# Kernel optimization log

Measured on AMD Instinct MI355X. Metric: run time of the kernel, lower is better.

Reference implementation:

```python
import jax, jax.numpy as jnp
import numpy as np

N = 4096

def setup_inputs() -> dict:
    key = jax.random.key(0)
    k1, k2, k3 = jax.random.split(key, 3)
    x = jax.random.normal(k1, (N, N), dtype=jnp.float32)
    # nn.Linear(N, N, bias=False) weight matrices, shape [out, in] = [N, N]
    s = 1.0 / np.sqrt(N)
    W_r = jax.random.uniform(k2, (N, N), dtype=jnp.float32, minval=-s, maxval=s)
    W_i = jax.random.uniform(k3, (N, N), dtype=jnp.float32, minval=-s, maxval=s)
    return {"x": x, "W_r": W_r, "W_i": W_i}

def reference(x, W_r, W_i):
    # Row pass: fft_in_rows[i] = Linear_real(x[i]) + 1j * Linear_imag(x[i])
    #   => R = x @ W_r^T + 1j * (x @ W_i^T)
    R_r = x @ W_r.T            # [N, N]
    R_i = x @ W_i.T            # [N, N]
    # Column pass: fft_in_cols[:, i] = fft_in_rows[:, i] @ (W_r + 1j W_i)
    #   => C = W^T @ R with W = W_r + 1j W_i (complex matmul in real arithmetic)
    C_r = W_r.T @ R_r - W_i.T @ R_i
    C_i = W_r.T @ R_i + W_i.T @ R_r
    # res = cat([real, imag], dim=1) -> [N, 2N]
    return jnp.concatenate([C_r, C_i], axis=1)
```

## Files before the change

kernel.cpp:

```cpp
#include <hip/hip_runtime.h>
#include <hip/hip_bf16.h>

#define NN 4096

typedef unsigned short u16;
using bf16x8 = __attribute__((ext_vector_type(8))) short;
using f32x4  = __attribute__((ext_vector_type(4))) float;
using u32x4  = __attribute__((ext_vector_type(4))) unsigned int;

__device__ inline u16 f2bf(float f) {
    union { float f; unsigned u; } c; c.f = f;
    unsigned r = (c.u + 0x7fffu + ((c.u >> 16) & 1u)) >> 16;
    return (u16)r;
}

__device__ inline void gld16(const void* g, void* l) {
    __builtin_amdgcn_global_load_lds(
        (const __attribute__((address_space(1))) void*)g,
        (__attribute__((address_space(3))) void*)l, 16, 0, 0);
}

__device__ inline bf16x8 negbf(bf16x8 v) {
    u32x4 u; __builtin_memcpy(&u, &v, 16);
    u ^= 0x80008000u;
    bf16x8 r; __builtin_memcpy(&r, &u, 16);
    return r;
}

__device__ inline void swz_tile(int bid, int& brow, int& bcol) {
    const int xcd   = bid & 7;
    const int local = bid >> 3;
    const int rr    = xcd >> 1;
    const int rc    = xcd & 1;
    brow = (rr * 8  + (local >> 4)) * 128;
    bcol = (rc * 16 + (local & 15)) * 128;
}

__global__ __launch_bounds__(256) void cvt_bf16(const float* __restrict__ s,
                                                u16* __restrict__ d) {
    size_t i = ((size_t)blockIdx.x * 256 + threadIdx.x) * 8;
    float4 v0 = *(const float4*)(s + i);
    float4 v1 = *(const float4*)(s + i + 4);
    bf16x8 o;
    o[0] = (short)f2bf(v0.x); o[1] = (short)f2bf(v0.y);
    o[2] = (short)f2bf(v0.z); o[3] = (short)f2bf(v0.w);
    o[4] = (short)f2bf(v1.x); o[5] = (short)f2bf(v1.y);
    o[6] = (short)f2bf(v1.z); o[7] = (short)f2bf(v1.w);
    *(bf16x8*)(d + i) = o;
}

__global__ __launch_bounds__(256) void tr_cvt(const float* __restrict__ s,
                                              u16* __restrict__ d) {
    __shared__ float t[32][33];
    int x  = blockIdx.x * 32 + threadIdx.x;
    int y0 = blockIdx.y * 32;
#pragma unroll
    for (int j = 0; j < 32; j += 8)
        t[threadIdx.y + j][threadIdx.x] = s[(size_t)(y0 + threadIdx.y + j) * NN + x];
    __syncthreads();
    int x2 = blockIdx.y * 32 + threadIdx.x;
    int y2 = blockIdx.x * 32;
#pragma unroll
    for (int j = 0; j < 32; j += 8)
        d[(size_t)(y2 + threadIdx.y + j) * NN + x2] = f2bf(t[threadIdx.x][threadIdx.y + j]);
}

#define P_BAR  __builtin_amdgcn_s_barrier()
#define P_LGKM do { asm volatile("s_waitcnt lgkmcnt(0)" ::: "memory"); \
                    __builtin_amdgcn_sched_barrier(0); } while (0)
#define P_VM0  do { asm volatile("s_waitcnt vmcnt(0)" ::: "memory"); \
                    __builtin_amdgcn_sched_barrier(0); } while (0)

#define CHAIN(AF, BF, ACC) do { \
    __builtin_amdgcn_s_setprio(1); \
    _Pragma("unroll") \
    for (int i_ = 0; i_ < 4; i_++) \
        _Pragma("unroll") \
        for (int j_ = 0; j_ < 4; j_++) \
            ACC[i_][j_] = __builtin_amdgcn_mfma_f32_16x16x32_bf16(AF[i_], BF[j_], ACC[i_][j_], 0, 0, 0); \
    __builtin_amdgcn_s_setprio(0); \
} while (0)

#define RD4(DST, CC, TILE, BASE) do { \
    _Pragma("unroll") \
    for (int i_ = 0; i_ < 4; i_++) \
        DST[i_] = *(const bf16x8*)&sm[CC][TILE][((BASE) + i_ * 16 + rl) * 32 + kg]; \
} while (0)


__global__ __launch_bounds__(256, 2) void gemm_pass1(
    const u16* __restrict__ Ar, const u16* __restrict__ Ai,
    const u16* __restrict__ B,
    u16* __restrict__ Cr, u16* __restrict__ Ci) {
    __shared__ u16 sm[2][3][4096];

    int brow, bcol;
    swz_tile(blockIdx.x, brow, bcol);

    const int tid  = threadIdx.x;
    const int lane = tid & 63;
    const int wid  = tid >> 6;
    const int wm   = (wid >> 1) * 64;
    const int wn   = (wid & 1) * 64;

    f32x4 accr[4][4] = {};
    f32x4 acci[4][4] = {};

    const int r0 = tid >> 2;
    const int lb = (tid & 3) ^ ((r0 >> 1) & 3);
    const size_t aoff0 = (size_t)(brow + r0) * NN + lb * 8;
    const size_t aoff1 = aoff0 + (size_t)64 * NN;
    const size_t boff0 = (size_t)(bcol + r0) * NN + lb * 8;
    const size_t boff1 = boff0 + (size_t)64 * NN;
    const int rl = lane & 15;
    const int kg = ((lane >> 4) ^ ((rl >> 1) & 3)) * 8;

#define T0(b, kk) gld16(Ar + aoff0 + (kk), &sm[b][0][tid * 8])
#define T1(b, kk) gld16(Ar + aoff1 + (kk), &sm[b][0][2048 + tid * 8])
#define T2(b, kk) gld16(Ai + aoff0 + (kk), &sm[b][1][tid * 8])
#define T3(b, kk) gld16(Ai + aoff1 + (kk), &sm[b][1][2048 + tid * 8])
#define T4(b, kk) gld16(B  + boff0 + (kk), &sm[b][2][tid * 8])
#define T5(b, kk) gld16(B  + boff1 + (kk), &sm[b][2][2048 + tid * 8])

#define KSTEP1(CC, NB, KN, DOSTG) do { \
    bf16x8 af[4], ag[4], bb[4]; \
    RD4(af, CC, 0, wm); RD4(bb, CC, 2, wn); \
    if (DOSTG) { T0(NB, KN); T1(NB, KN); T2(NB, KN); T3(NB, KN); } \
    P_BAR; P_LGKM; \
    CHAIN(af, bb, accr); \
    P_BAR; \
    RD4(ag, CC, 1, wm); \
    if (DOSTG) { T4(NB, KN); T5(NB, KN); } \
    P_BAR; P_LGKM; \
    CHAIN(ag, bb, acci); \
    if (DOSTG) P_VM0; \
    P_BAR; \
} while (0)

    T0(0, 0); T1(0, 0); T2(0, 0); T3(0, 0); T4(0, 0); T5(0, 0);
    P_VM0;
    P_BAR;
    for (int t = 0; t < NN / 32 - 1; ++t) {
        const int cc = t & 1, nb = cc ^ 1;
        KSTEP1(cc, nb, (size_t)(t + 1) * 32, 1);
    }
    KSTEP1(1, 0, 0, 0);

    const int rg = (lane >> 4) * 4;
#pragma unroll
    for (int i = 0; i < 4; i++)
#pragma unroll
        for (int j = 0; j < 4; j++) {
            int col = bcol + wn + j * 16 + rl;
#pragma unroll
            for (int r = 0; r < 4; r++) {
                int row = brow + wm + i * 16 + rg + r;
                Cr[(size_t)row * NN + col] = f2bf(accr[i][j][r]);
                Ci[(size_t)row * NN + col] = f2bf(acci[i][j][r]);
            }
        }
}

__global__ __launch_bounds__(256, 2) void gemm_pass2(
    const u16* __restrict__ Ar, const u16* __restrict__ Ai,
    const u16* __restrict__ Br, const u16* __restrict__ Bi,
    float* __restrict__ Out) {
    __shared__ u16 sm[2][4][4096];

    int brow, bcol;
    swz_tile(blockIdx.x, brow, bcol);

    const int tid  = threadIdx.x;
    const int lane = tid & 63;
    const int wid  = tid >> 6;
    const int wm   = (wid >> 1) * 64;
    const int wn   = (wid & 1) * 64;

    f32x4 accr[4][4] = {};
    f32x4 acci[4][4] = {};

    const int r0 = tid >> 2;
    const int lb = (tid & 3) ^ ((r0 >> 1) & 3);
    const size_t moff0 = (size_t)(brow + r0) * NN + lb * 8;
    const size_t moff1 = moff0 + (size_t)64 * NN;
    const size_t noff0 = (size_t)(bcol + r0) * NN + lb * 8;
    const size_t noff1 = noff0 + (size_t)64 * NN;
    const int rl = lane & 15;
    const int kg = ((lane >> 4) ^ ((rl >> 1) & 3)) * 8;

#define SL0(b, kk) gld16(Ar + moff0 + (kk), &sm[b][0][tid * 8])
#define SL1(b, kk) gld16(Ar + moff1 + (kk), &sm[b][0][2048 + tid * 8])
#define SL2(b, kk) gld16(Ai + moff0 + (kk), &sm[b][1][tid * 8])
#define SL3(b, kk) gld16(Ai + moff1 + (kk), &sm[b][1][2048 + tid * 8])
#define SL4(b, kk) gld16(Br + noff0 + (kk), &sm[b][2][tid * 8])
#define SL5(b, kk) gld16(Br + noff1 + (kk), &sm[b][2][2048 + tid * 8])
#define SL6(b, kk) gld16(Bi + noff0 + (kk), &sm[b][3][tid * 8])
#define SL7(b, kk) gld16(Bi + noff1 + (kk), &sm[b][3][2048 + tid * 8])

#define KSTEP2(CC, NB, KN, DOSTG) do { \
    bf16x8 ar[4], ai[4], br[4], bi[4]; \
     \
    RD4(ar, CC, 0, wm); RD4(bi, CC, 3, wn); \
    if (DOSTG) { SL0(NB, KN); SL1(NB, KN); SL2(NB, KN); } \
    P_BAR; P_LGKM; \
    CHAIN(ar, bi, acci); \
    P_BAR; \
     \
    RD4(br, CC, 2, wn); \
    if (DOSTG) { SL3(NB, KN); SL4(NB, KN); SL5(NB, KN); } \
    P_BAR; P_LGKM; \
    CHAIN(ar, br, accr); \
    P_BAR; \
     \
    RD4(ai, CC, 1, wm); \
    if (DOSTG) { SL6(NB, KN); SL7(NB, KN); } \
    P_BAR; P_LGKM; \
    CHAIN(ai, br, acci); \
    P_BAR; \
     \
    _Pragma("unroll") for (int i_ = 0; i_ < 4; i_++) ai[i_] = negbf(ai[i_]); \
    CHAIN(ai, bi, accr); \
    if (DOSTG) P_VM0; \
    P_BAR; \
} while (0)

    SL0(0, 0); SL1(0, 0); SL2(0, 0); SL3(0, 0);
    SL4(0, 0); SL5(0, 0); SL6(0, 0); SL7(0, 0);
    P_VM0;
    P_BAR;
    for (int t = 0; t < NN / 32 - 1; ++t) {
        const int cc = t & 1, nb = cc ^ 1;
        KSTEP2(cc, nb, (size_t)(t + 1) * 32, 1);
    }
    KSTEP2(1, 0, 0, 0);

    const int rg = (lane >> 4) * 4;
#pragma unroll
    for (int i = 0; i < 4; i++)
#pragma unroll
        for (int j = 0; j < 4; j++) {
            int col = bcol + wn + j * 16 + rl;
#pragma unroll
            for (int r = 0; r < 4; r++) {
                int row = brow + wm + i * 16 + rg + r;
                Out[(size_t)row * (2 * NN) + col]      = accr[i][j][r];
                Out[(size_t)row * (2 * NN) + NN + col] = acci[i][j][r];
            }
        }
}

extern "C" void kernel_launch(void* const* d_in, const int* in_sizes, int n_in,
                              void* d_out, int out_size, void* d_ws, size_t ws_size,
                              hipStream_t stream) {
    const float* x  = (const float*)d_in[0];
    const float* Wr = (const float*)d_in[1];
    const float* Wi = (const float*)d_in[2];
    float* out = (float*)d_out;

    const size_t SZ = (size_t)NN * NN;
    u16* ws  = (u16*)d_ws;
    u16* xb  = ws;
    u16* Wrb = ws + SZ;
    u16* Wib = ws + 2 * SZ;
    u16* Rtr = ws + 3 * SZ;
    u16* Rti = ws + 4 * SZ;

    cvt_bf16<<<8192, 256, 0, stream>>>(x,  xb);
    cvt_bf16<<<8192, 256, 0, stream>>>(Wr, Wrb);
    cvt_bf16<<<8192, 256, 0, stream>>>(Wi, Wib);

    gemm_pass1<<<1024, 256, 0, stream>>>(Wrb, Wib, xb, Rtr, Rti);

    u16* WrT = xb;
    u16* WiT = Wrb;
    tr_cvt<<<dim3(128, 128), dim3(32, 8), 0, stream>>>(Wr, WrT);
    tr_cvt<<<dim3(128, 128), dim3(32, 8), 0, stream>>>(Wi, WiT);

    gemm_pass2<<<1024, 256, 0, stream>>>(WrT, WiT, Rtr, Rti, out);
}
```

Baseline: 770.3 us.

## Switch GEMM inner loops to 32x32x16 bf16 MFMA with fewer barrier phases

Both GEMM passes replace the 16x16x32 MFMA tiling with 32x32x16 MFMA, so each wave computes its 64x64 tile as 2x2 32x32 blocks. This means fewer MFMA issues and fewer LDS fragment reads per k-step. The k-step is also restructured so all next-stage global->LDS loads are issued up front and some barrier phases are merged, with pass2 computing two products after one sync. The epilogue is rewritten for the 32x32 accumulator layout. This raises register pressure, especially in pass2 where four fragment sets are live at once, which could hurt occupancy at two blocks per CU.

```diff
diff --git a/kernel.cpp b/kernel.cpp
--- a/kernel.cpp
+++ b/kernel.cpp
@@ -5,7 +5,7 @@
 
 typedef unsigned short u16;
 using bf16x8 = __attribute__((ext_vector_type(8))) short;
-using f32x4  = __attribute__((ext_vector_type(4))) float;
+using f32x16 = __attribute__((ext_vector_type(16))) float;
 using u32x4  = __attribute__((ext_vector_type(4))) unsigned int;
 
 __device__ inline u16 f2bf(float f) {
@@ -71,20 +71,21 @@
 #define P_VM0  do { asm volatile("s_waitcnt vmcnt(0)" ::: "memory"); \
                     __builtin_amdgcn_sched_barrier(0); } while (0)
 
-#define CHAIN(AF, BF, ACC) do { \
-    __builtin_amdgcn_s_setprio(1); \
-    _Pragma("unroll") \
-    for (int i_ = 0; i_ < 4; i_++) \
-        _Pragma("unroll") \
-        for (int j_ = 0; j_ < 4; j_++) \
-            ACC[i_][j_] = __builtin_amdgcn_mfma_f32_16x16x32_bf16(AF[i_], BF[j_], ACC[i_][j_], 0, 0, 0); \
-    __builtin_amdgcn_s_setprio(0); \
-} while (0)
-
-#define RD4(DST, CC, TILE, BASE) do { \
-    _Pragma("unroll") \
-    for (int i_ = 0; i_ < 4; i_++) \
-        DST[i_] = *(const bf16x8*)&sm[CC][TILE][((BASE) + i_ * 16 + rl) * 32 + kg]; \
+#define MF32(a_, b_, c_) __builtin_amdgcn_mfma_f32_32x32x16_bf16(a_, b_, c_, 0, 0, 0)
+
+#define CHAIN32(A, B, ACC) do { \
+    ACC[0][0] = MF32(A##00, B##00, ACC[0][0]); ACC[0][0] = MF32(A##01, B##01, ACC[0][0]); \
+    ACC[0][1] = MF32(A##00, B##10, ACC[0][1]); ACC[0][1] = MF32(A##01, B##11, ACC[0][1]); \
+    ACC[1][0] = MF32(A##10, B##00, ACC[1][0]); ACC[1][0] = MF32(A##11, B##01, ACC[1][0]); \
+    ACC[1][1] = MF32(A##10, B##10, ACC[1][1]); ACC[1][1] = MF32(A##11, B##11, ACC[1][1]); \
+} while (0)
+
+#define RDF(D, CC, TILE, BASE) do { \
+    const int rA_ = ((BASE) + l31) * 32, rB_ = ((BASE) + 32 + l31) * 32; \
+    D##00 = *(const bf16x8*)&sm[CC][TILE][rA_ + ((kh ^ sxor) * 8)]; \
+    D##01 = *(const bf16x8*)&sm[CC][TILE][rA_ + (((2 + kh) ^ sxor) * 8)]; \
+    D##10 = *(const bf16x8*)&sm[CC][TILE][rB_ + ((kh ^ sxor) * 8)]; \
+    D##11 = *(const bf16x8*)&sm[CC][TILE][rB_ + (((2 + kh) ^ sxor) * 8)]; \
 } while (0)
 
 
@@ -102,9 +103,12 @@
     const int wid  = tid >> 6;
     const int wm   = (wid >> 1) * 64;
     const int wn   = (wid & 1) * 64;
-
-    f32x4 accr[4][4] = {};
-    f32x4 acci[4][4] = {};
+    const int l31  = lane & 31;
+    const int kh   = lane >> 5;
+    const int sxor = (l31 >> 1) & 3;
+
+    f32x16 accr[2][2] = {};
+    f32x16 acci[2][2] = {};
 
     const int r0 = tid >> 2;
     const int lb = (tid & 3) ^ ((r0 >> 1) & 3);
@@ -112,8 +116,6 @@
     const size_t aoff1 = aoff0 + (size_t)64 * NN;
     const size_t boff0 = (size_t)(bcol + r0) * NN + lb * 8;
     const size_t boff1 = boff0 + (size_t)64 * NN;
-    const int rl = lane & 15;
-    const int kg = ((lane >> 4) ^ ((rl >> 1) & 3)) * 8;
 
 #define T0(b, kk) gld16(Ar + aoff0 + (kk), &sm[b][0][tid * 8])
 #define T1(b, kk) gld16(Ar + aoff1 + (kk), &sm[b][0][2048 + tid * 8])
@@ -123,16 +125,21 @@
 #define T5(b, kk) gld16(B  + boff1 + (kk), &sm[b][2][2048 + tid * 8])
 
 #define KSTEP1(CC, NB, KN, DOSTG) do { \
-    bf16x8 af[4], ag[4], bb[4]; \
-    RD4(af, CC, 0, wm); RD4(bb, CC, 2, wn); \
-    if (DOSTG) { T0(NB, KN); T1(NB, KN); T2(NB, KN); T3(NB, KN); } \
-    P_BAR; P_LGKM; \
-    CHAIN(af, bb, accr); \
-    P_BAR; \
-    RD4(ag, CC, 1, wm); \
-    if (DOSTG) { T4(NB, KN); T5(NB, KN); } \
-    P_BAR; P_LGKM; \
-    CHAIN(ag, bb, acci); \
+    bf16x8 ar00, ar01, ar10, ar11, ai00, ai01, ai10, ai11; \
+    bf16x8 bx00, bx01, bx10, bx11; \
+    RDF(ar, CC, 0, wm); RDF(bx, CC, 2, wn); \
+    if (DOSTG) { T0(NB, KN); T1(NB, KN); T2(NB, KN); \
+                 T3(NB, KN); T4(NB, KN); T5(NB, KN); } \
+    P_BAR; P_LGKM; \
+    __builtin_amdgcn_s_setprio(1); \
+    CHAIN32(ar, bx, accr); \
+    __builtin_amdgcn_s_setprio(0); \
+    P_BAR; \
+    RDF(ai, CC, 1, wm); \
+    P_BAR; P_LGKM; \
+    __builtin_amdgcn_s_setprio(1); \
+    CHAIN32(ai, bx, acci); \
+    __builtin_amdgcn_s_setprio(0); \
     if (DOSTG) P_VM0; \
     P_BAR; \
 } while (0)
@@ -146,17 +153,16 @@
     }
     KSTEP1(1, 0, 0, 0);
 
-    const int rg = (lane >> 4) * 4;
-#pragma unroll
-    for (int i = 0; i < 4; i++)
-#pragma unroll
-        for (int j = 0; j < 4; j++) {
-            int col = bcol + wn + j * 16 + rl;
-#pragma unroll
-            for (int r = 0; r < 4; r++) {
-                int row = brow + wm + i * 16 + rg + r;
-                Cr[(size_t)row * NN + col] = f2bf(accr[i][j][r]);
-                Ci[(size_t)row * NN + col] = f2bf(acci[i][j][r]);
+#pragma unroll
+    for (int i = 0; i < 2; i++)
+#pragma unroll
+        for (int j = 0; j < 2; j++) {
+            const int col = bcol + wn + j * 32 + l31;
+#pragma unroll
+            for (int e = 0; e < 16; e++) {
+                const int row = brow + wm + i * 32 + (e & 3) + 8 * (e >> 2) + 4 * kh;
+                Cr[(size_t)row * NN + col] = f2bf(accr[i][j][e]);
+                Ci[(size_t)row * NN + col] = f2bf(acci[i][j][e]);
             }
         }
 }
@@ -175,9 +181,12 @@
     const int wid  = tid >> 6;
     const int wm   = (wid >> 1) * 64;
     const int wn   = (wid & 1) * 64;
-
-    f32x4 accr[4][4] = {};
-    f32x4 acci[4][4] = {};
+    const int l31  = lane & 31;
+    const int kh   = lane >> 5;
+    const int sxor = (l31 >> 1) & 3;
+
+    f32x16 accr[2][2] = {};
+    f32x16 acci[2][2] = {};
 
     const int r0 = tid >> 2;
     const int lb = (tid & 3) ^ ((r0 >> 1) & 3);
@@ -185,8 +194,6 @@
     const size_t moff1 = moff0 + (size_t)64 * NN;
     const size_t noff0 = (size_t)(bcol + r0) * NN + lb * 8;
     const size_t noff1 = noff0 + (size_t)64 * NN;
-    const int rl = lane & 15;
-    const int kg = ((lane >> 4) ^ ((rl >> 1) & 3)) * 8;
 
 #define SL0(b, kk) gld16(Ar + moff0 + (kk), &sm[b][0][tid * 8])
 #define SL1(b, kk) gld16(Ar + moff1 + (kk), &sm[b][0][2048 + tid * 8])
@@ -198,28 +205,26 @@
 #define SL7(b, kk) gld16(Bi + noff1 + (kk), &sm[b][3][2048 + tid * 8])
 
 #define KSTEP2(CC, NB, KN, DOSTG) do { \
-    bf16x8 ar[4], ai[4], br[4], bi[4]; \
+    bf16x8 ar00, ar01, ar10, ar11, ai00, ai01, ai10, ai11; \
+    bf16x8 br00, br01, br10, br11, bi00, bi01, bi10, bi11; \
      \
-    RD4(ar, CC, 0, wm); RD4(bi, CC, 3, wn); \
-    if (DOSTG) { SL0(NB, KN); SL1(NB, KN); SL2(NB, KN); } \
-    P_BAR; P_LGKM; \
-    CHAIN(ar, bi, acci); \
+    RDF(ar, CC, 0, wm); RDF(br, CC, 2, wn); RDF(bi, CC, 3, wn); \
+    if (DOSTG) { SL0(NB, KN); SL1(NB, KN); SL2(NB, KN); SL3(NB, KN); \
+                 SL4(NB, KN); SL5(NB, KN); SL6(NB, KN); SL7(NB, KN); } \
+    P_BAR; P_LGKM; \
+    __builtin_amdgcn_s_setprio(1); \
+    CHAIN32(ar, bi, acci); \
+    CHAIN32(ar, br, accr); \
+    __builtin_amdgcn_s_setprio(0); \
     P_BAR; \
      \
-    RD4(br, CC, 2, wn); \
-    if (DOSTG) { SL3(NB, KN); SL4(NB, KN); SL5(NB, KN); } \
-    P_BAR; P_LGKM; \
-    CHAIN(ar, br, accr); \
-    P_BAR; \
-     \
-    RD4(ai, CC, 1, wm); \
-    if (DOSTG) { SL6(NB, KN); SL7(NB, KN); } \
-    P_BAR; P_LGKM; \
-    CHAIN(ai, br, acci); \
-    P_BAR; \
-     \
-    _Pragma("unroll") for (int i_ = 0; i_ < 4; i_++) ai[i_] = negbf(ai[i_]); \
-    CHAIN(ai, bi, accr); \
+    RDF(ai, CC, 1, wm); \
+    P_BAR; P_LGKM; \
+    __builtin_amdgcn_s_setprio(1); \
+    CHAIN32(ai, br, acci); \
+    ai00 = negbf(ai00); ai01 = negbf(ai01); ai10 = negbf(ai10); ai11 = negbf(ai11); \
+    CHAIN32(ai, bi, accr); \
+    __builtin_amdgcn_s_setprio(0); \
     if (DOSTG) P_VM0; \
     P_BAR; \
 } while (0)
@@ -234,17 +239,16 @@
     }
     KSTEP2(1, 0, 0, 0);
 
-    const int rg = (lane >> 4) * 4;
-#pragma unroll
-    for (int i = 0; i < 4; i++)
-#pragma unroll
-        for (int j = 0; j < 4; j++) {
-            int col = bcol + wn + j * 16 + rl;
-#pragma unroll
-            for (int r = 0; r < 4; r++) {
-                int row = brow + wm + i * 16 + rg + r;
-                Out[(size_t)row * (2 * NN) + col]      = accr[i][j][r];
-                Out[(size_t)row * (2 * NN) + NN + col] = acci[i][j][r];
+#pragma unroll
+    for (int i = 0; i < 2; i++)
+#pragma unroll
+        for (int j = 0; j < 2; j++) {
+            const int col = bcol + wn + j * 32 + l31;
+#pragma unroll
+            for (int e = 0; e < 16; e++) {
+                const int row = brow + wm + i * 32 + (e & 3) + 8 * (e >> 2) + 4 * kh;
+                Out[(size_t)row * (2 * NN) + col]      = accr[i][j][e];
+                Out[(size_t)row * (2 * NN) + NN + col] = acci[i][j][e];
             }
         }
 }
```

Result: slower. 847.4 us (+10.0%).
